# Kernel optimization log

Measured on AMD Instinct MI355X. Metric: run time of the kernel, lower is better.

## Reference

```python
import jax, jax.numpy as jnp
import numpy as np
import math

DIMS = [2048, 1024, 512, 4096]
NH, DK, DV = 16, 64, 64
BS = 8192
D_MODEL = NH * DK  # 1024


def setup_inputs() -> dict:
    key = jax.random.key(0)
    ks = jax.random.split(key, 3 * len(DIMS) + 5)
    inp = {"input_data": jax.random.normal(ks[0], (BS, sum(DIMS)), jnp.float32)}
    ki = 1
    for i, d in enumerate(DIMS):
        inp[f"wq{i}"] = jax.random.normal(ks[ki], (NH * DK, d), jnp.float32) * 0.02; ki += 1
        inp[f"wk{i}"] = jax.random.normal(ks[ki], (NH * DK, d), jnp.float32) * 0.02; ki += 1
        inp[f"wv{i}"] = jax.random.normal(ks[ki], (NH * DV, d), jnp.float32) * 0.02; ki += 1
    inp["fc_w"] = jax.random.normal(ks[ki], (NH * DV, NH * DV), jnp.float32) * 0.02; ki += 1
    inp["fc_b"] = jax.random.normal(ks[ki], (NH * DV,), jnp.float32) * 0.02; ki += 1
    inp["ln_g"] = jnp.ones((NH * DV,), jnp.float32)
    inp["ln_b"] = jnp.zeros((NH * DV,), jnp.float32)
    return inp


def _forward(input_data, wqs, wks, wvs, fc_w, fc_b, ln_g, ln_b):
    bs = input_data.shape[0]
    M = len(DIMS)
    offs = np.cumsum([0] + DIMS)
    # per-modality projections; stack into [bs, M, NH*D]
    xs = [input_data[:, offs[i]:offs[i + 1]] for i in range(M)]
    q = jnp.stack([x @ w.T for x, w in zip(xs, wqs)], axis=1)  # [bs, M, NH*DK]
    k = jnp.stack([x @ w.T for x, w in zip(xs, wks)], axis=1)
    v = jnp.stack([x @ w.T for x, w in zip(xs, wvs)], axis=1)  # [bs, M, NH*DV]
    residual = v  # v.transpose(1,2).view == original stacked v
    qh = q.reshape(bs, M, NH, DK).transpose(0, 2, 1, 3)  # [bs, NH, M, DK]
    kh = k.reshape(bs, M, NH, DK).transpose(0, 2, 1, 3)
    vh = v.reshape(bs, M, NH, DV).transpose(0, 2, 1, 3)
    scores = jnp.einsum('bhqd,bhkd->bhqk', qh, kh) / math.sqrt(DK)
    attn = jax.nn.softmax(scores, axis=-1)  # [bs, NH, M, M]
    ctx = jnp.einsum('bhqk,bhkd->bhqd', attn, vh)  # [bs, NH, M, DV]
    ctx = ctx.transpose(0, 2, 1, 3).reshape(bs, M, NH * DV)
    out = ctx @ fc_w.T + fc_b  # dropout is identity (p=0 / eval)
    out = out + residual
    mu = jnp.mean(out, axis=-1, keepdims=True)
    var = jnp.var(out, axis=-1, keepdims=True)
    out = (out - mu) / jnp.sqrt(var + 1e-6) * ln_g + ln_b
    return out, attn


def reference(input_data, wq0, wk0, wv0, wq1, wk1, wv1, wq2, wk2, wv2,
              wq3, wk3, wv3, fc_w, fc_b, ln_g, ln_b):
    wqs = [wq0, wq1, wq2, wq3]
    wks = [wk0, wk1, wk2, wk3]
    wvs = [wv0, wv1, wv2, wv3]
    return _forward(input_data, wqs, wks, wvs, fc_w, fc_b, ln_g, ln_b)
```

## Files before the change

kernel.cpp:

```cpp
#include <hip/hip_runtime.h>


typedef unsigned short u16;
typedef short short8 __attribute__((ext_vector_type(8)));
typedef float f32x4 __attribute__((ext_vector_type(4)));

__device__ __forceinline__ u16 f2bf(float f) {
  unsigned u = __builtin_bit_cast(unsigned, f);
  u += 0x7FFFu + ((u >> 16) & 1u);
  return (u16)(u >> 16);
}
__device__ __forceinline__ float bf2f(u16 s) {
  return __builtin_bit_cast(float, ((unsigned)s) << 16);
}

__device__ __forceinline__ void gload16(const u16* g, u16* l) {
  __builtin_amdgcn_global_load_lds(
      (const __attribute__((address_space(1))) void*)g,
      (__attribute__((address_space(3))) void*)l, 16, 0, 0);
}

#define CFENCE asm volatile("" ::: "memory")

struct CArgs {
  const float* src[14];
  unsigned long dst[14];
  int blk0[14];
  int n4[14];
};

__global__ __launch_bounds__(256) void convall(CArgs a, u16* __restrict__ wsb) {
  int blk = blockIdx.x;
  int s = 0;
#pragma unroll
  for (int i = 1; i < 14; ++i) s = (blk >= a.blk0[i]) ? i : s;
  int li = (blk - a.blk0[s]) * 256 + threadIdx.x;
  if (li < a.n4[s]) {
    float4 v = ((const float4*)a.src[s])[li];
    ushort4 o;
    o.x = f2bf(v.x); o.y = f2bf(v.y); o.z = f2bf(v.z); o.w = f2bf(v.w);
    ((ushort4*)(wsb + a.dst[s]))[li] = o;
  }
}

template <int MODE>
__global__ __launch_bounds__(512, 1)
void gemm8(const u16* __restrict__ Abase, int lda,
           const u16* __restrict__ Wbase, u16* __restrict__ Cq,
           float* __restrict__ Cf, const float* __restrict__ bias,
           const u16* __restrict__ resid) {
  __shared__ __align__(16) u16 lds[65536];

  const int tid = threadIdx.x;
  const int w = tid >> 6, lane = tid & 63;
  const int lr = lane & 15, lk = lane >> 4;
  const int wm = w >> 2, wn = w & 3;

  int K, nt, bx, by, coff;
  const u16 *A, *B;
  if (MODE == 0) {
    int seg = blockIdx.x / 384;
    int r = blockIdx.x % 384;
    r = (r & 7) * 48 + (r >> 3);
    bx = r % 12; by = r / 12;
    K = 4096 >> seg; nt = 128 >> seg;
    int xo, wo, mod;
    switch (seg) {
      case 0:  xo = 3584; wo = 11010048; mod = 3; break;
      case 1:  xo = 0;    wo = 0;        mod = 0; break;
      case 2:  xo = 2048; wo = 6291456;  mod = 1; break;
      default: xo = 3072; wo = 9437184;  mod = 2; break;
    }
    coff = mod * 3072;
    A = Abase + xo;
    B = Wbase + wo;
  } else {
    int r = (blockIdx.x & 7) * 64 + (blockIdx.x >> 3);
    bx = r & 3; by = r >> 2;
    K = 1024; nt = 32; coff = 0;
    A = Abase; B = Wbase;
  }
  const size_t brow = (size_t)by * 256;
  const int bcol = bx * 256;
  const u16* Ab = A + brow * (size_t)lda;
  const u16* Bb = B + (size_t)bcol * (size_t)K;

  const int stg_row = lane >> 2;
  const int stg_k = ((lane & 3) ^ ((lane >> 3) & 3)) * 8;
  const int fso = (lk ^ ((lr >> 1) & 3)) * 8;

  f32x4 acc[8][4];
#pragma unroll
  for (int i = 0; i < 8; ++i)
#pragma unroll
    for (int j = 0; j < 4; ++j) acc[i][j] = (f32x4){0.f, 0.f, 0.f, 0.f};

  auto stageA = [&](int p) {
    const int bb = (p & 3) * 16384;
    const int k0 = p * 32;
#pragma unroll
    for (int h = 0; h < 2; ++h)
      gload16(Ab + (size_t)(h * 128 + w * 16 + stg_row) * lda + k0 + stg_k,
              (u16*)&lds[bb + h * 4096 + w * 512]);
  };
  auto stageB = [&](int p) {
    const int bb = (p & 3) * 16384 + 8192;
    const int k0 = p * 32;
#pragma unroll
    for (int h = 0; h < 2; ++h)
      gload16(Bb + (size_t)(h * 128 + w * 16 + stg_row) * (size_t)K + k0 + stg_k,
              (u16*)&lds[bb + h * 4096 + w * 512]);
  };

  stageA(0); stageB(0);
  stageA(1); stageB(1);
  stageA(2); stageB(2);
  asm volatile("s_waitcnt vmcnt(8)" ::: "memory");
  __builtin_amdgcn_s_barrier();
  CFENCE;

#pragma unroll 1
  for (int t = 0; t < nt; ++t) {
    const int bb = (t & 3) * 16384;
    if (t + 3 < nt) { stageA(t + 3); stageB(t + 3); }
    CFENCE;
    short8 bfr[4], af[8];
#pragma unroll
    for (int ni = 0; ni < 4; ++ni)
      bfr[ni] = *(const short8*)&lds[bb + 8192 + (wn * 64 + ni * 16 + lr) * 32 + fso];
#pragma unroll
    for (int mi = 0; mi < 8; ++mi)
      af[mi] = *(const short8*)&lds[bb + (wm * 128 + mi * 16 + lr) * 32 + fso];
    __builtin_amdgcn_s_setprio(1);
#pragma unroll
    for (int mi = 0; mi < 8; ++mi)
#pragma unroll
      for (int ni = 0; ni < 4; ++ni)
        acc[mi][ni] = __builtin_amdgcn_mfma_f32_16x16x32_bf16(
            af[mi], bfr[ni], acc[mi][ni], 0, 0, 0);
    __builtin_amdgcn_s_setprio(0);
    CFENCE;
    if (t + 1 < nt) {
      if (t + 3 < nt)      asm volatile("s_waitcnt vmcnt(8)" ::: "memory");
      else if (t + 2 < nt) asm volatile("s_waitcnt vmcnt(4)" ::: "memory");
      else                 asm volatile("s_waitcnt vmcnt(0)" ::: "memory");
      __builtin_amdgcn_s_barrier();
      CFENCE;
    }
  }

  if (MODE == 0) {
#pragma unroll
    for (int mi = 0; mi < 8; ++mi)
#pragma unroll
      for (int ni = 0; ni < 4; ++ni) {
        const int c = coff + bcol + wn * 64 + ni * 16 + lr;
#pragma unroll
        for (int j = 0; j < 4; ++j) {
          size_t r = brow + wm * 128 + mi * 16 + lk * 4 + j;
          Cq[r * 12288 + c] = f2bf(acc[mi][ni][j]);
        }
      }
  } else {
#pragma unroll
    for (int mi = 0; mi < 8; ++mi)
#pragma unroll
      for (int ni = 0; ni < 4; ++ni) {
        const int c = bcol + wn * 64 + ni * 16 + lr;
        const float bs = bias[c];
#pragma unroll
        for (int j = 0; j < 4; ++j) {
          size_t r = brow + wm * 128 + mi * 16 + lk * 4 + j;
          size_t ridx = (r >> 2) * 12288 + (r & 3) * 3072 + 2048 + c;
          Cf[r * 1024 + c] = acc[mi][ni][j] + bs + bf2f(resid[ridx]);
        }
      }
  }
}

__global__ __launch_bounds__(256) void attn_k(const u16* __restrict__ qkv,
                                              u16* __restrict__ ctxb,
                                              float* __restrict__ attn_out) {
  const int tid = threadIdx.x;
  const int l = tid & 63;
  const int wg = blockIdx.x * 4 + (tid >> 6);
  const int b = wg >> 2;
  const int h0 = (wg & 3) << 2;
  const size_t base = (size_t)b * 12288 + h0 * 64 + l * 4;

  float q[4][4], k[4][4], v[4][4];
#pragma unroll
  for (int m = 0; m < 4; ++m) {
    ushort4 uq = *(const ushort4*)(qkv + base + m * 3072);
    ushort4 uk = *(const ushort4*)(qkv + base + m * 3072 + 1024);
    ushort4 uv = *(const ushort4*)(qkv + base + m * 3072 + 2048);
    q[m][0] = bf2f(uq.x); q[m][1] = bf2f(uq.y); q[m][2] = bf2f(uq.z); q[m][3] = bf2f(uq.w);
    k[m][0] = bf2f(uk.x); k[m][1] = bf2f(uk.y); k[m][2] = bf2f(uk.z); k[m][3] = bf2f(uk.w);
    v[m][0] = bf2f(uv.x); v[m][1] = bf2f(uv.y); v[m][2] = bf2f(uv.z); v[m][3] = bf2f(uv.w);
  }

  float s[16];
#pragma unroll
  for (int i = 0; i < 4; ++i)
#pragma unroll
    for (int j = 0; j < 4; ++j) {
      float acc = q[i][0] * k[j][0];
      acc += q[i][1] * k[j][1];
      acc += q[i][2] * k[j][2];
      acc += q[i][3] * k[j][3];
      s[i * 4 + j] = acc;
    }
#pragma unroll
  for (int off = 1; off < 16; off <<= 1) {
#pragma unroll
    for (int t = 0; t < 16; ++t) s[t] += __shfl_xor(s[t], off);
  }

  float a[16];
#pragma unroll
  for (int i = 0; i < 4; ++i) {
    float s0 = s[i * 4 + 0] * 0.125f, s1 = s[i * 4 + 1] * 0.125f;
    float s2 = s[i * 4 + 2] * 0.125f, s3 = s[i * 4 + 3] * 0.125f;
    float m = fmaxf(fmaxf(s0, s1), fmaxf(s2, s3));
    float e0 = __expf(s0 - m), e1 = __expf(s1 - m);
    float e2 = __expf(s2 - m), e3 = __expf(s3 - m);
    float inv = 1.0f / (e0 + e1 + e2 + e3);
    a[i * 4 + 0] = e0 * inv; a[i * 4 + 1] = e1 * inv;
    a[i * 4 + 2] = e2 * inv; a[i * 4 + 3] = e3 * inv;
  }

#pragma unroll
  for (int i = 0; i < 4; ++i) {
    float c0 = a[i*4+0]*v[0][0] + a[i*4+1]*v[1][0] + a[i*4+2]*v[2][0] + a[i*4+3]*v[3][0];
    float c1 = a[i*4+0]*v[0][1] + a[i*4+1]*v[1][1] + a[i*4+2]*v[2][1] + a[i*4+3]*v[3][1];
    float c2 = a[i*4+0]*v[0][2] + a[i*4+1]*v[1][2] + a[i*4+2]*v[2][2] + a[i*4+3]*v[3][2];
    float c3 = a[i*4+0]*v[0][3] + a[i*4+1]*v[1][3] + a[i*4+2]*v[2][3] + a[i*4+3]*v[3][3];
    ushort4 o;
    o.x = f2bf(c0); o.y = f2bf(c1); o.z = f2bf(c2); o.w = f2bf(c3);
    *(ushort4*)(ctxb + (size_t)b * 4096 + i * 1024 + h0 * 64 + l * 4) = o;
  }

  int sel = l & 15;
  float val = a[0];
#pragma unroll
  for (int t = 1; t < 16; ++t) val = (sel == t) ? a[t] : val;
  attn_out[(size_t)b * 256 + h0 * 16 + l] = val;
}

__global__ __launch_bounds__(256) void ln_k(const float* __restrict__ pre,
                                            const float* __restrict__ g,
                                            const float* __restrict__ b,
                                            float* __restrict__ out) {
  int row = blockIdx.x;
  int tid = threadIdx.x;
  const float4 x = *(const float4*)(pre + (size_t)row * 1024 + tid * 4);
  float s = x.x + x.y + x.z + x.w;
  float s2 = x.x * x.x + x.y * x.y + x.z * x.z + x.w * x.w;
#pragma unroll
  for (int off = 32; off; off >>= 1) {
    s += __shfl_xor(s, off);
    s2 += __shfl_xor(s2, off);
  }
  __shared__ float r1[4], r2[4];
  int w = tid >> 6, lane = tid & 63;
  if (lane == 0) { r1[w] = s; r2[w] = s2; }
  __syncthreads();
  s = r1[0] + r1[1] + r1[2] + r1[3];
  s2 = r2[0] + r2[1] + r2[2] + r2[3];
  float mu = s * (1.0f / 1024.0f);
  float inv = rsqrtf(s2 * (1.0f / 1024.0f) - mu * mu + 1e-6f);
  float4 gv = *(const float4*)(g + tid * 4);
  float4 bv = *(const float4*)(b + tid * 4);
  float4 o;
  o.x = (x.x - mu) * inv * gv.x + bv.x;
  o.y = (x.y - mu) * inv * gv.y + bv.y;
  o.z = (x.z - mu) * inv * gv.z + bv.z;
  o.w = (x.w - mu) * inv * gv.w + bv.w;
  *(float4*)(out + (size_t)row * 1024 + tid * 4) = o;
}

extern "C" void kernel_launch(void* const* d_in, const int* in_sizes, int n_in,
                              void* d_out, int out_size, void* d_ws,
                              size_t ws_size, hipStream_t stream) {
  const float* fcb = (const float*)d_in[14];
  const float* lng = (const float*)d_in[15];
  const float* lnb = (const float*)d_in[16];

  u16* wsb = (u16*)d_ws;
  u16* xb = wsb;
  u16* wb = xb + 62914560;
  u16* qkv = wb + 24641536;
  u16* ctxb = qkv + 100663296;
  float* pre = (float*)d_ws;
  float* outp = (float*)d_out;
  float* attn_out = outp + 33554432;

  static const unsigned long woff[13] = {
      0,        2097152,  4194304,
      6291456,  7340032,  8388608,
      9437184,  9961472,  10485760,
      11010048, 15204352, 19398656,
      23592960};
  static const int wn4[13] = {524288, 524288, 524288, 262144, 262144, 262144,
                              131072, 131072, 131072, 1048576, 1048576, 1048576,
                              262144};

  CArgs ca;
  ca.src[0] = (const float*)d_in[0];
  ca.dst[0] = 0;
  ca.n4[0] = 62914560 / 4;
  ca.blk0[0] = 0;
  int nb = ca.n4[0] / 256;
  for (int i = 0; i < 13; ++i) {
    ca.src[i + 1] = (const float*)d_in[1 + i];
    ca.dst[i + 1] = 62914560ul + woff[i];
    ca.n4[i + 1] = wn4[i];
    ca.blk0[i + 1] = nb;
    nb += (wn4[i] + 255) / 256;
  }
  convall<<<dim3(nb), 256, 0, stream>>>(ca, wsb);

  gemm8<0><<<dim3(1536), 512, 0, stream>>>(xb, 7680, wb, qkv, nullptr, nullptr,
                                           nullptr);

  attn_k<<<dim3(8192), 256, 0, stream>>>(qkv, ctxb, attn_out);

  gemm8<1><<<dim3(512), 512, 0, stream>>>(ctxb, 1024, wb + 23592960, nullptr,
                                          pre, fcb, qkv);

  ln_k<<<dim3(32768), 256, 0, stream>>>(pre, lng, lnb, outp);
}
```

Before: 659.1 us.

## Software-pipeline LDS fragment loads with register double buffering in bf16 GEMM

Restructures the GEMM main loop so that the next k-step's A and B fragments are read from LDS into registers while the current step's MFMAs run. B fragments are double-buffered, A is split into two halves, and global-to-LDS prefetch is deepened to four stages, with the loop unrolled by two. The aim is to hide LDS read latency and make waits and barriers cheaper. The launch bound is also raised to two blocks per CU. That caps registers per thread and could force spills of the 128-float accumulator plus the extra fragment buffers. Since the kernel already uses 128KB of LDS, a second block probably cannot be resident anyway.

```diff
diff --git a/kernel.cpp b/kernel.cpp
--- a/kernel.cpp
+++ b/kernel.cpp
@@ -44,7 +44,7 @@
 }
 
 template <int MODE>
-__global__ __launch_bounds__(512, 1)
+__global__ __launch_bounds__(512, 2)
 void gemm8(const u16* __restrict__ Abase, int lda,
            const u16* __restrict__ Wbase, u16* __restrict__ Cq,
            float* __restrict__ Cf, const float* __restrict__ bias,
@@ -95,58 +95,78 @@
 #pragma unroll
     for (int j = 0; j < 4; ++j) acc[i][j] = (f32x4){0.f, 0.f, 0.f, 0.f};
 
-  auto stageA = [&](int p) {
+  auto stage = [&](int p) {
     const int bb = (p & 3) * 16384;
     const int k0 = p * 32;
 #pragma unroll
     for (int h = 0; h < 2; ++h)
       gload16(Ab + (size_t)(h * 128 + w * 16 + stg_row) * lda + k0 + stg_k,
               (u16*)&lds[bb + h * 4096 + w * 512]);
-  };
-  auto stageB = [&](int p) {
-    const int bb = (p & 3) * 16384 + 8192;
-    const int k0 = p * 32;
 #pragma unroll
     for (int h = 0; h < 2; ++h)
       gload16(Bb + (size_t)(h * 128 + w * 16 + stg_row) * (size_t)K + k0 + stg_k,
-              (u16*)&lds[bb + h * 4096 + w * 512]);
+              (u16*)&lds[bb + 8192 + h * 4096 + w * 512]);
   };
 
-  stageA(0); stageB(0);
-  stageA(1); stageB(1);
-  stageA(2); stageB(2);
-  asm volatile("s_waitcnt vmcnt(8)" ::: "memory");
+  auto ldA = [&](int t, int half, short8* dst) {
+    const int bb = (t & 3) * 16384;
+#pragma unroll
+    for (int mi = 0; mi < 4; ++mi)
+      dst[mi] = *(const short8*)
+          &lds[bb + (wm * 128 + (half * 4 + mi) * 16 + lr) * 32 + fso];
+  };
+  auto ldB = [&](int t, short8* dst) {
+    const int bb = (t & 3) * 16384;
+#pragma unroll
+    for (int ni = 0; ni < 4; ++ni)
+      dst[ni] = *(const short8*)
+          &lds[bb + 8192 + (wn * 64 + ni * 16 + lr) * 32 + fso];
+  };
+
+  stage(0); stage(1); stage(2); stage(3);
+  asm volatile("s_waitcnt vmcnt(12)" ::: "memory");
   __builtin_amdgcn_s_barrier();
   CFENCE;
-
-#pragma unroll 1
-  for (int t = 0; t < nt; ++t) {
-    const int bb = (t & 3) * 16384;
-    if (t + 3 < nt) { stageA(t + 3); stageB(t + 3); }
-    CFENCE;
-    short8 bfr[4], af[8];
-#pragma unroll
-    for (int ni = 0; ni < 4; ++ni)
-      bfr[ni] = *(const short8*)&lds[bb + 8192 + (wn * 64 + ni * 16 + lr) * 32 + fso];
-#pragma unroll
-    for (int mi = 0; mi < 8; ++mi)
-      af[mi] = *(const short8*)&lds[bb + (wm * 128 + mi * 16 + lr) * 32 + fso];
-    __builtin_amdgcn_s_setprio(1);
-#pragma unroll
-    for (int mi = 0; mi < 8; ++mi)
-#pragma unroll
-      for (int ni = 0; ni < 4; ++ni)
-        acc[mi][ni] = __builtin_amdgcn_mfma_f32_16x16x32_bf16(
-            af[mi], bfr[ni], acc[mi][ni], 0, 0, 0);
-    __builtin_amdgcn_s_setprio(0);
-    CFENCE;
-    if (t + 1 < nt) {
-      if (t + 3 < nt)      asm volatile("s_waitcnt vmcnt(8)" ::: "memory");
-      else if (t + 2 < nt) asm volatile("s_waitcnt vmcnt(4)" ::: "memory");
-      else                 asm volatile("s_waitcnt vmcnt(0)" ::: "memory");
+  short8 Alo[4], Ahi[4], Bp0[4], Bp1[4];
+  ldA(0, 0, Alo);
+  ldB(0, Bp0);
+  ldA(0, 1, Ahi);
+
+  auto step = [&](int t, short8* Bc, short8* Bn) {
+    int c = nt - 1 - t;
+    if (c > 3) c = 3;
+    if (c > 0) {
+      asm volatile("s_waitcnt lgkmcnt(0)" ::: "memory");
+      if (c == 3)      asm volatile("s_waitcnt vmcnt(8)" ::: "memory");
+      else if (c == 2) asm volatile("s_waitcnt vmcnt(4)" ::: "memory");
+      else             asm volatile("s_waitcnt vmcnt(0)" ::: "memory");
       __builtin_amdgcn_s_barrier();
       CFENCE;
     }
+    __builtin_amdgcn_s_setprio(1);
+#pragma unroll
+    for (int mi = 0; mi < 4; ++mi)
+#pragma unroll
+      for (int ni = 0; ni < 4; ++ni)
+        acc[mi][ni] = __builtin_amdgcn_mfma_f32_16x16x32_bf16(
+            Alo[mi], Bc[ni], acc[mi][ni], 0, 0, 0);
+    if (t + 1 < nt) { ldA(t + 1, 0, Alo); ldB(t + 1, Bn); }
+    if (t + 4 < nt) stage(t + 4);
+#pragma unroll
+    for (int mi = 0; mi < 4; ++mi)
+#pragma unroll
+      for (int ni = 0; ni < 4; ++ni)
+        acc[mi + 4][ni] = __builtin_amdgcn_mfma_f32_16x16x32_bf16(
+            Ahi[mi], Bc[ni], acc[mi + 4][ni], 0, 0, 0);
+    if (t + 1 < nt) ldA(t + 1, 1, Ahi);
+    __builtin_amdgcn_s_setprio(0);
+    CFENCE;
+  };
+
+#pragma unroll 1
+  for (int t = 0; t < nt; t += 2) {
+    step(t, Bp0, Bp1);
+    step(t + 1, Bp1, Bp0);
   }
 
   if (MODE == 0) {
```

After: 669.8 us. Within noise of the previous version (+1.6%).
